# Kernel optimization log

Hardware: AMD Instinct MI355X
Metric: run time of the kernel (lower is better)

Reference implementation:

```python
import jax, jax.numpy as jnp
import numpy as np

D = 16      # input_dim (state dimension)
H = 64      # hidden width
B = 32768   # batch size


def setup_inputs() -> dict:
    key = jax.random.key(0)
    ks = jax.random.split(key, 16)
    inp = {
        "ts": jnp.arange(3, dtype=jnp.float32),          # output times [0, 1, 2]
        "x0": jax.random.normal(ks[0], (B, D), jnp.float32),
    }
    dims = [(D, H), (H, H), (H, H), (H, D)]
    i = 1
    for l, (din, dout) in enumerate(dims):
        inp[f"W{l}"] = jax.random.normal(ks[i], (din, dout), jnp.float32) / np.sqrt(din).astype(np.float32)
        inp[f"b{l}"] = jnp.zeros((dout,), jnp.float32)
        inp[f"g{l}"] = jax.random.normal(ks[i + 1], (dout,), jnp.float32) * 0.1   # hyper_gate weight (Linear(1,dout))
        inp[f"gb{l}"] = jnp.zeros((dout,), jnp.float32)                            # hyper_gate bias
        inp[f"hb{l}"] = jax.random.normal(ks[i + 2], (dout,), jnp.float32) * 0.1   # hyper_bias weight (no bias)
        i += 3
    return inp


def reference(ts, x0,
              W0, b0, g0, gb0, hb0,
              W1, b1, g1, gb1, hb1,
              W2, b2, g2, gb2, hb2,
              W3, b3, g3, gb3, hb3):
    layers = [(W0, b0, g0, gb0, hb0), (W1, b1, g1, gb1, hb1),
              (W2, b2, g2, gb2, hb2), (W3, b3, g3, gb3, hb3)]
    n_layers = len(layers)

    def odenet(t, x):
        # ConcatSquashLinear: (x@W + b) * sigmoid(t*g + gb) + t*hb, tanh between layers
        h = x
        for l, (W, b, g, gb, hb) in enumerate(layers):
            h = (h @ W + b) * jax.nn.sigmoid(t * g + gb) + t * hb
            if l < n_layers - 1:
                h = jnp.tanh(h)
        return h

    def odefunc(t, z):
        # z: [B, D+2]; last two channels accumulate log-det and kinetic energy
        x = z[:, :D]
        f = lambda xx: odenet(t, xx)
        dx = f(x)
        # exact divergence = trace of Jacobian, via D forward-mode JVPs
        eye = jnp.eye(D, dtype=x.dtype)
        Jv = jax.vmap(lambda e: jax.jvp(f, (x,), (jnp.broadcast_to(e, x.shape),))[1])(eye)  # [D, B, D]
        dl = jnp.einsum('ibi->b', Jv)                  # trace per sample
        dv = 0.5 * jnp.sum(dx * dx, axis=1)            # kinetic energy density
        return jnp.concatenate([dx, dl[:, None], dv[:, None]], axis=1)

    z0 = jnp.pad(x0, ((0, 0), (0, 2)))  # F.pad(x0, (0,2)) with zeros

    def rk4_step(z, t_pair):
        t0, t1 = t_pair
        h = t1 - t0
        k1 = odefunc(t0, z)
        k2 = odefunc(t0 + 0.5 * h, z + 0.5 * h * k1)
        k3 = odefunc(t0 + 0.5 * h, z + 0.5 * h * k2)
        k4 = odefunc(t1, z + h * k3)
        zn = z + (h / 6.0) * (k1 + 2.0 * k2 + 2.0 * k3 + k4)
        return zn, zn

    _, zs_tail = jax.lax.scan(rk4_step, z0, (ts[:-1], ts[1:]))
    zs = jnp.concatenate([z0[None], zs_tail], axis=0)   # [T, B, D+2]

    xs = zs[:, :, :-2]
    log_det = zs[-1, :, -2]
    loss_L = jnp.abs(zs[-1, :, -1])
    return xs, log_det, loss_L, jnp.zeros_like(loss_L)
```

## Files before the change

kernel.cpp:

```cpp
#include <hip/hip_runtime.h>

#define NB 32768
#define DD 16
#define HH 64
#define EPB 16

typedef __attribute__((ext_vector_type(8))) short short8;
typedef __attribute__((ext_vector_type(2))) float f32x2;
typedef __attribute__((ext_vector_type(4))) float f32x4;
typedef __attribute__((ext_vector_type(4))) unsigned uint4v;

union Frag { short8 s; uint4v u; unsigned d[4]; };

struct Params {
  const float *ts, *x0;
  const float *W0,*b0,*g0,*gb0,*hb0;
  const float *W1,*b1,*g1,*gb1,*hb1;
  const float *W2,*b2,*g2,*gb2,*hb2;
  const float *W3,*b3,*g3,*gb3,*hb3;
  float *out;
};

__device__ __forceinline__ float bfs(unsigned short u){
  return __uint_as_float(((unsigned)u)<<16);
}
__device__ __forceinline__ unsigned short f2bf(float f){
  unsigned u=__float_as_uint(f);
  return (unsigned short)((u + 0x7FFFu + ((u>>16)&1u))>>16);
}
__device__ __forceinline__ unsigned pk2bf(float lo, float hi){
  unsigned a=__float_as_uint(lo)+0x8000u;
  unsigned b=__float_as_uint(hi)+0x8000u;
  return __builtin_amdgcn_perm(b, a, 0x07060302u);
}
__device__ __forceinline__ unsigned short f2bf1(float f){
  return (unsigned short)((__float_as_uint(f)+0x8000u)>>16);
}
__device__ __forceinline__ float sigm(float u){
  return __builtin_amdgcn_rcpf(1.0f+__builtin_amdgcn_exp2f(-1.44269504f*u));
}
#define WV() __builtin_amdgcn_wave_barrier()
#define MFMA(A,B,C) __builtin_amdgcn_mfma_f32_16x16x32_bf16((A),(B),(C),0,0,0)

__device__ __forceinline__ void fwd_epi(const f32x4& c, float tcur,
    const float4 sc,
    unsigned short* __restrict__ hdst, unsigned short* __restrict__ sdst,
    int jw, int q)
{
  const float gate = sigm(tcur*sc.x+sc.y);
  const float gk   = gate*2.88539008f;
  const float tbk  = (tcur*sc.z)*2.88539008f;
  const float g4   = 4.0f*gate;
  const f32x2 c01={c[0],c[1]}, c23={c[2],c[3]};
  const f32x2 pre01 = c01*gk + tbk;
  const f32x2 pre23 = c23*gk + tbk;
  const f32x2 e01={__builtin_amdgcn_exp2f(pre01[0]),__builtin_amdgcn_exp2f(pre01[1])};
  const f32x2 e23={__builtin_amdgcn_exp2f(pre23[0]),__builtin_amdgcn_exp2f(pre23[1])};
  const f32x2 d01=e01+1.0f, d23=e23+1.0f;
  const f32x2 rc01={__builtin_amdgcn_rcpf(d01[0]),__builtin_amdgcn_rcpf(d01[1])};
  const f32x2 rc23={__builtin_amdgcn_rcpf(d23[0]),__builtin_amdgcn_rcpf(d23[1])};
  const f32x2 th01 = rc01*-2.0f + 1.0f;
  const f32x2 th23 = rc23*-2.0f + 1.0f;
  const f32x2 om01 = 1.0f - rc01, om23 = 1.0f - rc23;
  const f32x2 sv01 = (rc01*g4)*om01, sv23 = (rc23*g4)*om23;
  const int el0=q*4;
  hdst[(el0+0)*72+jw]=f2bf1(th01[0]);
  hdst[(el0+1)*72+jw]=f2bf1(th01[1]);
  hdst[(el0+2)*72+jw]=f2bf1(th23[0]);
  hdst[(el0+3)*72+jw]=f2bf1(th23[1]);
  sdst[(el0+0)*72+jw]=f2bf1(sv01[0]);
  sdst[(el0+1)*72+jw]=f2bf1(sv01[1]);
  sdst[(el0+2)*72+jw]=f2bf1(sv23[0]);
  sdst[(el0+3)*72+jw]=f2bf1(sv23[1]);
}

__device__ __forceinline__ void fwd_epi0(const f32x4& c, float tcur,
    const float4 sc,
    unsigned short* __restrict__ hdst, float* __restrict__ sdstf,
    int jw, int q)
{
  const float gate = sigm(tcur*sc.x+sc.y);
  const float gk   = gate*2.88539008f;
  const float tbk  = (tcur*sc.z)*2.88539008f;
  const float g4   = 4.0f*gate;
  const f32x2 c01={c[0],c[1]}, c23={c[2],c[3]};
  const f32x2 pre01 = c01*gk + tbk;
  const f32x2 pre23 = c23*gk + tbk;
  const f32x2 e01={__builtin_amdgcn_exp2f(pre01[0]),__builtin_amdgcn_exp2f(pre01[1])};
  const f32x2 e23={__builtin_amdgcn_exp2f(pre23[0]),__builtin_amdgcn_exp2f(pre23[1])};
  const f32x2 d01=e01+1.0f, d23=e23+1.0f;
  const f32x2 rc01={__builtin_amdgcn_rcpf(d01[0]),__builtin_amdgcn_rcpf(d01[1])};
  const f32x2 rc23={__builtin_amdgcn_rcpf(d23[0]),__builtin_amdgcn_rcpf(d23[1])};
  const f32x2 th01 = rc01*-2.0f + 1.0f;
  const f32x2 th23 = rc23*-2.0f + 1.0f;
  const f32x2 om01 = 1.0f - rc01, om23 = 1.0f - rc23;
  const f32x2 sv01 = (rc01*g4)*om01, sv23 = (rc23*g4)*om23;
  const int el0=q*4;
  hdst[(el0+0)*72+jw]=f2bf1(th01[0]);
  hdst[(el0+1)*72+jw]=f2bf1(th01[1]);
  hdst[(el0+2)*72+jw]=f2bf1(th23[0]);
  hdst[(el0+3)*72+jw]=f2bf1(th23[1]);
  sdstf[(el0+0)*72+jw]=sv01[0];
  sdstf[(el0+1)*72+jw]=sv01[1];
  sdstf[(el0+2)*72+jw]=sv23[0];
  sdstf[(el0+3)*72+jw]=sv23[1];
}

__global__ __launch_bounds__(256,3) void traj_kernel(Params p){
  __shared__ __align__(16) float w0f[DD][72];
  __shared__ __align__(16) float w3tt[HH][20];
  __shared__ __align__(16) unsigned short w0t[HH][16];
  __shared__ __align__(16) unsigned short b3f[2][64][8];
  __shared__ __align__(16) unsigned short w2tf[2][4][64][8];
  __shared__ __align__(16) float4 lscA[3][64];
  __shared__ __align__(16) float4 lsc3[16];
  __shared__ __align__(16) unsigned short xh[DD][16];
  __shared__ __align__(16) unsigned short xl[DD][16];
  __shared__ __align__(16) unsigned short hbh[2][EPB][72];
  __shared__ __align__(16) float sb0f[EPB][72];
  __shared__ __align__(16) unsigned short sb12[2][EPB][72];
  __shared__ __align__(16) float sig3w[4][DD];
  __shared__ __align__(16) float dxs[4][4][17];
  __shared__ __align__(16) unsigned short vt[4][DD][72];

  const int tid = threadIdx.x;
  const int e   = tid>>4;
  const int a   = tid&15;
  const int wv  = tid>>6;
  const int lane= tid&63;
  const int m   = lane&15;
  const int q   = lane>>4;
  const int b   = blockIdx.x*EPB + e;
  const int jw  = wv*16 + m;

  short8 f1fr[2], f2fr[2];
  short8 b1fr[2][4];
  {
    #pragma unroll
    for(int kk=0;kk<2;++kk){
      #pragma unroll
      for(int j=0;j<8;++j){
        const int k=kk*32+q*8+j;
        f1fr[kk][j]=(short)f2bf(p.W1[k*HH+jw]);
        f2fr[kk][j]=(short)f2bf(p.W2[k*HH+jw]);
      }
      #pragma unroll
      for(int nt=0;nt<4;++nt){
        #pragma unroll
        for(int j=0;j<8;++j){
          const int k=kk*32+q*8+j;
          b1fr[kk][nt][j]=(short)f2bf(p.W1[k*HH+4*m+nt]);
        }
      }
    }
  }

  for(int idx=tid; idx<DD*HH; idx+=256) w0f[idx>>6][idx&63]=p.W0[idx];
  for(int idx=tid; idx<HH*DD; idx+=256) w3tt[idx>>4][idx&15]=p.W3[idx];
  for(int idx=tid; idx<HH*16; idx+=256){
    const int c_=idx>>4, k=idx&15;
    w0t[c_][k]=f2bf(p.W0[k*HH+c_]);
  }
  for(int idx=tid; idx<1024; idx+=256){
    const int kk=idx>>9, ln=(idx>>3)&63, j=idx&7;
    const int k=kk*32+(ln>>4)*8+j;
    b3f[kk][ln][j]=f2bf(p.W3[k*DD+(ln&15)]);
  }
  for(int idx=tid; idx<4096; idx+=256){
    const int j=idx&7, ln=(idx>>3)&63, nt=(idx>>9)&3, kk=idx>>11;
    const int k=kk*32+((ln>>4)&3)*8+j;
    w2tf[kk][nt][ln][j]=f2bf(p.W2[k*HH+4*(ln&15)+nt]);
  }
  if(tid<64)            lscA[0][tid]    =make_float4(p.g0[tid],p.gb0[tid],p.hb0[tid],p.b0[tid]);
  else if(tid<128)      lscA[1][tid-64] =make_float4(p.g1[tid-64],p.gb1[tid-64],p.hb1[tid-64],p.b1[tid-64]);
  else if(tid<192)      lscA[2][tid-128]=make_float4(p.g2[tid-128],p.gb2[tid-128],p.hb2[tid-128],p.b2[tid-128]);
  else if(tid<208)      lsc3[tid-192]   =make_float4(p.g3[tid-192],p.gb3[tid-192],p.hb3[tid-192],p.b3[tid-192]);
  __syncthreads();

  float zbx = p.x0[b*DD+a];
  p.out[b*DD+a]=zbx;
  float trp[4]={0.f,0.f,0.f,0.f};
  float dvp=0.f;

  #pragma unroll 1
  for(int step=0; step<2; ++step){
    const float t0=p.ts[step], t1=p.ts[step+1];
    const float hs=t1-t0;
    float dzx=0.f;
    float zwx=zbx;
    #pragma unroll 1
    for(int stage=0; stage<4; ++stage){
      const float cin=(stage==0)?0.f:((stage==3)?1.f:0.5f);
      const float tcur=t0+cin*hs;
      const float wg=(stage==0||stage==3)?1.f:2.f;
      const float fs=hs*(1.f/6.f)*wg;
      const float fs5=0.5f*fs;

      {
        const unsigned ux=__float_as_uint(zwx);
        xh[e][a]=(unsigned short)(ux>>16);
        xl[e][a]=f2bf1(zwx-__uint_as_float(ux&0xFFFF0000u));
      }
      __syncthreads();

      float4 sc0=lscA[0][jw];
      f32x4 c={sc0.w,sc0.w,sc0.w,sc0.w};
      {
        short8 f0fr=short8{0,0,0,0,0,0,0,0};
        short8 ah=f0fr, al=f0fr;
        if(q<2){
          f0fr=*reinterpret_cast<const short8*>(&w0t[jw][q*8]);
          ah  =*reinterpret_cast<const short8*>(&xh[m][q*8]);
          al  =*reinterpret_cast<const short8*>(&xl[m][q*8]);
        }
        c=MFMA(ah,f0fr,c); c=MFMA(al,f0fr,c);
      }
      fwd_epi0(c,tcur,sc0,&hbh[0][0][0],&sb0f[0][0],jw,q);
      __syncthreads();

      float4 sc1=lscA[1][jw];
      c=f32x4{sc1.w,sc1.w,sc1.w,sc1.w};
      #pragma unroll
      for(int kk=0;kk<2;++kk){
        const short8 ah=*reinterpret_cast<const short8*>(&hbh[0][m][kk*32+q*8]);
        c=MFMA(ah,f1fr[kk],c);
      }
      fwd_epi(c,tcur,sc1,&hbh[1][0][0],&sb12[0][0][0],jw,q);
      __syncthreads();

      float4 sc2=lscA[2][jw];
      c=f32x4{sc2.w,sc2.w,sc2.w,sc2.w};
      #pragma unroll
      for(int kk=0;kk<2;++kk){
        const short8 ah=*reinterpret_cast<const short8*>(&hbh[1][m][kk*32+q*8]);
        c=MFMA(ah,f2fr[kk],c);
      }
      fwd_epi(c,tcur,sc2,&hbh[0][0][0],&sb12[1][0][0],jw,q);
      __syncthreads();

      float4 sc3=lsc3[m];
      c=f32x4{sc3.w,sc3.w,sc3.w,sc3.w};
      #pragma unroll
      for(int kk=0;kk<2;++kk){
        const short8 bf3=*reinterpret_cast<const short8*>(&b3f[kk][lane][0]);
        const short8 ah=*reinterpret_cast<const short8*>(&hbh[0][m][kk*32+q*8]);
        c=MFMA(ah,bf3,c);
      }
      const float gate3=sigm(tcur*sc3.x+sc3.y);
      const float tb3=tcur*sc3.z;
      if(q==wv){
        #pragma unroll
        for(int r=0;r<4;++r)
          dxs[wv][r][m]=c[r]*gate3+tb3;
      }
      if(q==0) sig3w[wv][m]=gate3;
      WV();
      const float dxk=dxs[wv][q][m];
      dvp += fs5*dxk*dxk;

      f32x2 tf2[4][2];
      {
        const f32x4 sg4=*reinterpret_cast<const f32x4*>(&sig3w[wv][q*4]);
        const f32x2 sgA={sg4[0],sg4[1]}, sgB={sg4[2],sg4[3]};
        #pragma unroll
        for(int nt=0;nt<4;++nt){
          const f32x4 w4=*reinterpret_cast<const f32x4*>(&w3tt[4*m+nt][q*4]);
          tf2[nt][0]=sgA*f32x2{w4[0],w4[1]};
          tf2[nt][1]=sgB*f32x2{w4[2],w4[3]};
        }
      }

      #pragma unroll
      for(int el=0; el<4; ++el){
        const int ee=wv*4+el;
        Frag a0[2];
        #pragma unroll
        for(int kk=0;kk<2;++kk){
          const f32x4 wa=*reinterpret_cast<const f32x4*>(&w0f[m][kk*32+q*8]);
          const f32x4 wb=*reinterpret_cast<const f32x4*>(&w0f[m][kk*32+q*8+4]);
          const f32x4 sa=*reinterpret_cast<const f32x4*>(&sb0f[ee][kk*32+q*8]);
          const f32x4 sc_=*reinterpret_cast<const f32x4*>(&sb0f[ee][kk*32+q*8+4]);
          a0[kk].d[0]=pk2bf(wa[0]*sa[0], wa[1]*sa[1]);
          a0[kk].d[1]=pk2bf(wa[2]*sa[2], wa[3]*sa[3]);
          a0[kk].d[2]=pk2bf(wb[0]*sc_[0], wb[1]*sc_[1]);
          a0[kk].d[3]=pk2bf(wb[2]*sc_[2], wb[3]*sc_[3]);
        }
        #pragma unroll
        for(int np=0; np<2; ++np){
          f32x4 cA={0,0,0,0}, cB={0,0,0,0};
          #pragma unroll
          for(int kk=0;kk<2;++kk){
            cA=MFMA(a0[kk].s,b1fr[kk][2*np  ],cA);
            cB=MFMA(a0[kk].s,b1fr[kk][2*np+1],cB);
          }
          const unsigned s1d=*reinterpret_cast<const unsigned*>(&sb12[0][ee][4*m+2*np]);
          const float sA_=__uint_as_float(s1d<<16), sB_=__uint_as_float(s1d&0xFFFF0000u);
          const f32x4 prA=cA*sA_, prB=cB*sB_;
          #pragma unroll
          for(int r=0;r<4;++r)
            *reinterpret_cast<unsigned*>(&vt[wv][q*4+r][4*m+2*np])=pk2bf(prA[r],prB[r]);
        }
        WV();
        short8 a2[2];
        #pragma unroll
        for(int kk=0;kk<2;++kk)
          a2[kk]=*reinterpret_cast<const short8*>(&vt[wv][m][kk*32+q*8]);
        float tr=0.f;
        #pragma unroll
        for(int np=0; np<2; ++np){
          f32x4 cA={0,0,0,0}, cB={0,0,0,0};
          #pragma unroll
          for(int kk=0;kk<2;++kk){
            const short8 bA=*reinterpret_cast<const short8*>(&w2tf[kk][2*np  ][lane][0]);
            const short8 bB=*reinterpret_cast<const short8*>(&w2tf[kk][2*np+1][lane][0]);
            cA=MFMA(a2[kk],bA,cA);
            cB=MFMA(a2[kk],bB,cB);
          }
          const unsigned s2d=*reinterpret_cast<const unsigned*>(&sb12[1][ee][4*m+2*np]);
          const float s20=__uint_as_float(s2d<<16), s21=__uint_as_float(s2d&0xFFFF0000u);
          const f32x2 tA = f32x2{cA[0],cA[1]}*tf2[2*np  ][0] + f32x2{cA[2],cA[3]}*tf2[2*np  ][1];
          const f32x2 tB = f32x2{cB[0],cB[1]}*tf2[2*np+1][0] + f32x2{cB[2],cB[3]}*tf2[2*np+1][1];
          tr += (tA[0]+tA[1])*s20 + (tB[0]+tB[1])*s21;
        }
        trp[el] += fs*tr;
        WV();
      }

      dzx += fs*dxk;
      const float cn=(stage==2)?1.f:0.5f;
      if(stage<3) zwx=zbx+cn*hs*dxk;
    }
    zbx += dzx;
    p.out[(step+1)*(NB*DD)+b*DD+a]=zbx;
  }

  #pragma unroll
  for(int el=0; el<4; ++el){
    float v=trp[el];
    #pragma unroll
    for(int mk=32;mk>=1;mk>>=1) v+=__shfl_xor(v,mk,64);
    if(lane==el) p.out[3*NB*DD + blockIdx.x*EPB + wv*4 + el]=v;
  }
  {
    float v=dvp;
    #pragma unroll
    for(int mk=8;mk>=1;mk>>=1) v+=__shfl_xor(v,mk,16);
    if(a==0){
      p.out[3*NB*DD+NB+b]=fabsf(v);
      p.out[3*NB*DD+2*NB+b]=0.f;
    }
  }
}

extern "C" void kernel_launch(void* const* d_in, const int* in_sizes, int n_in,
                              void* d_out, int out_size, void* d_ws, size_t ws_size,
                              hipStream_t stream){
  Params p;
  p.ts  = (const float*)d_in[0];
  p.x0  = (const float*)d_in[1];
  p.W0  = (const float*)d_in[2];  p.b0 =(const float*)d_in[3];
  p.g0  = (const float*)d_in[4];  p.gb0=(const float*)d_in[5];  p.hb0=(const float*)d_in[6];
  p.W1  = (const float*)d_in[7];  p.b1 =(const float*)d_in[8];
  p.g1  = (const float*)d_in[9];  p.gb1=(const float*)d_in[10]; p.hb1=(const float*)d_in[11];
  p.W2  = (const float*)d_in[12]; p.b2 =(const float*)d_in[13];
  p.g2  = (const float*)d_in[14]; p.gb2=(const float*)d_in[15]; p.hb2=(const float*)d_in[16];
  p.W3  = (const float*)d_in[17]; p.b3 =(const float*)d_in[18];
  p.g3  = (const float*)d_in[19]; p.gb3=(const float*)d_in[20]; p.hb3=(const float*)d_in[21];
  p.out = (float*)d_out;
  hipLaunchKernelGGL(traj_kernel, dim3(NB/EPB), dim3(256), 0, stream, p);
}
```

Baseline: 238.0 us.

## Hold W2/W3 MFMA fragments in registers and alias activation and JVP LDS buffers

Moves the W2-transpose and W3 B-fragments from shared memory into per-lane registers, which removes the LDS reads inside the per-element JVP loop. The hbh activation buffers and the vt JVP buffer now share one region, with an extra block barrier added before the JVP phase to make the reuse safe. Row padding of w0f and sb0f changes from 72 to 76 floats to reduce bank conflicts. Launch bounds drop from 3 to 2 blocks per CU so the extra registers fit, which lowers occupancy.

```diff
diff --git a/kernel.cpp b/kernel.cpp
--- a/kernel.cpp
+++ b/kernel.cpp
@@ -100,28 +100,25 @@
   hdst[(el0+1)*72+jw]=f2bf1(th01[1]);
   hdst[(el0+2)*72+jw]=f2bf1(th23[0]);
   hdst[(el0+3)*72+jw]=f2bf1(th23[1]);
-  sdstf[(el0+0)*72+jw]=sv01[0];
-  sdstf[(el0+1)*72+jw]=sv01[1];
-  sdstf[(el0+2)*72+jw]=sv23[0];
-  sdstf[(el0+3)*72+jw]=sv23[1];
-}
-
-__global__ __launch_bounds__(256,3) void traj_kernel(Params p){
-  __shared__ __align__(16) float w0f[DD][72];
+  sdstf[(el0+0)*76+jw]=sv01[0];
+  sdstf[(el0+1)*76+jw]=sv01[1];
+  sdstf[(el0+2)*76+jw]=sv23[0];
+  sdstf[(el0+3)*76+jw]=sv23[1];
+}
+
+__global__ __launch_bounds__(256,2) void traj_kernel(Params p){
+  __shared__ __align__(16) float w0f[DD][76];
   __shared__ __align__(16) float w3tt[HH][20];
   __shared__ __align__(16) unsigned short w0t[HH][16];
-  __shared__ __align__(16) unsigned short b3f[2][64][8];
-  __shared__ __align__(16) unsigned short w2tf[2][4][64][8];
   __shared__ __align__(16) float4 lscA[3][64];
   __shared__ __align__(16) float4 lsc3[16];
   __shared__ __align__(16) unsigned short xh[DD][16];
   __shared__ __align__(16) unsigned short xl[DD][16];
-  __shared__ __align__(16) unsigned short hbh[2][EPB][72];
-  __shared__ __align__(16) float sb0f[EPB][72];
+  __shared__ __align__(16) unsigned short hvt[4][DD][72];
+  __shared__ __align__(16) float sb0f[EPB][76];
   __shared__ __align__(16) unsigned short sb12[2][EPB][72];
   __shared__ __align__(16) float sig3w[4][DD];
   __shared__ __align__(16) float dxs[4][4][17];
-  __shared__ __align__(16) unsigned short vt[4][DD][72];
 
   const int tid = threadIdx.x;
   const int e   = tid>>4;
@@ -135,6 +132,8 @@
 
   short8 f1fr[2], f2fr[2];
   short8 b1fr[2][4];
+  short8 w2r[2][4];
+  short8 b3r[2];
   {
     #pragma unroll
     for(int kk=0;kk<2;++kk){
@@ -143,6 +142,7 @@
         const int k=kk*32+q*8+j;
         f1fr[kk][j]=(short)f2bf(p.W1[k*HH+jw]);
         f2fr[kk][j]=(short)f2bf(p.W2[k*HH+jw]);
+        b3r[kk][j]=(short)f2bf(p.W3[k*DD+m]);
       }
       #pragma unroll
       for(int nt=0;nt<4;++nt){
@@ -150,6 +150,7 @@
         for(int j=0;j<8;++j){
           const int k=kk*32+q*8+j;
           b1fr[kk][nt][j]=(short)f2bf(p.W1[k*HH+4*m+nt]);
+          w2r[kk][nt][j]=(short)f2bf(p.W2[k*HH+4*m+nt]);
         }
       }
     }
@@ -160,16 +161,6 @@
   for(int idx=tid; idx<HH*16; idx+=256){
     const int c_=idx>>4, k=idx&15;
     w0t[c_][k]=f2bf(p.W0[k*HH+c_]);
-  }
-  for(int idx=tid; idx<1024; idx+=256){
-    const int kk=idx>>9, ln=(idx>>3)&63, j=idx&7;
-    const int k=kk*32+(ln>>4)*8+j;
-    b3f[kk][ln][j]=f2bf(p.W3[k*DD+(ln&15)]);
-  }
-  for(int idx=tid; idx<4096; idx+=256){
-    const int j=idx&7, ln=(idx>>3)&63, nt=(idx>>9)&3, kk=idx>>11;
-    const int k=kk*32+((ln>>4)&3)*8+j;
-    w2tf[kk][nt][ln][j]=f2bf(p.W2[k*HH+4*(ln&15)+nt]);
   }
   if(tid<64)            lscA[0][tid]    =make_float4(p.g0[tid],p.gb0[tid],p.hb0[tid],p.b0[tid]);
   else if(tid<128)      lscA[1][tid-64] =make_float4(p.g1[tid-64],p.gb1[tid-64],p.hb1[tid-64],p.b1[tid-64]);
@@ -215,36 +206,35 @@
         }
         c=MFMA(ah,f0fr,c); c=MFMA(al,f0fr,c);
       }
-      fwd_epi0(c,tcur,sc0,&hbh[0][0][0],&sb0f[0][0],jw,q);
+      fwd_epi0(c,tcur,sc0,&hvt[0][0][0],&sb0f[0][0],jw,q);
       __syncthreads();
 
       float4 sc1=lscA[1][jw];
       c=f32x4{sc1.w,sc1.w,sc1.w,sc1.w};
       #pragma unroll
       for(int kk=0;kk<2;++kk){
-        const short8 ah=*reinterpret_cast<const short8*>(&hbh[0][m][kk*32+q*8]);
+        const short8 ah=*reinterpret_cast<const short8*>(&hvt[0][m][kk*32+q*8]);
         c=MFMA(ah,f1fr[kk],c);
       }
-      fwd_epi(c,tcur,sc1,&hbh[1][0][0],&sb12[0][0][0],jw,q);
+      fwd_epi(c,tcur,sc1,&hvt[1][0][0],&sb12[0][0][0],jw,q);
       __syncthreads();
 
       float4 sc2=lscA[2][jw];
       c=f32x4{sc2.w,sc2.w,sc2.w,sc2.w};
       #pragma unroll
       for(int kk=0;kk<2;++kk){
-        const short8 ah=*reinterpret_cast<const short8*>(&hbh[1][m][kk*32+q*8]);
+        const short8 ah=*reinterpret_cast<const short8*>(&hvt[1][m][kk*32+q*8]);
         c=MFMA(ah,f2fr[kk],c);
       }
-      fwd_epi(c,tcur,sc2,&hbh[0][0][0],&sb12[1][0][0],jw,q);
+      fwd_epi(c,tcur,sc2,&hvt[0][0][0],&sb12[1][0][0],jw,q);
       __syncthreads();
 
       float4 sc3=lsc3[m];
       c=f32x4{sc3.w,sc3.w,sc3.w,sc3.w};
       #pragma unroll
       for(int kk=0;kk<2;++kk){
-        const short8 bf3=*reinterpret_cast<const short8*>(&b3f[kk][lane][0]);
-        const short8 ah=*reinterpret_cast<const short8*>(&hbh[0][m][kk*32+q*8]);
-        c=MFMA(ah,bf3,c);
+        const short8 ah=*reinterpret_cast<const short8*>(&hvt[0][m][kk*32+q*8]);
+        c=MFMA(ah,b3r[kk],c);
       }
       const float gate3=sigm(tcur*sc3.x+sc3.y);
       const float tb3=tcur*sc3.z;
@@ -269,6 +259,8 @@
           tf2[nt][1]=sgB*f32x2{w4[2],w4[3]};
         }
       }
+
+      __syncthreads();
 
       #pragma unroll
       for(int el=0; el<4; ++el){
@@ -298,23 +290,21 @@
           const f32x4 prA=cA*sA_, prB=cB*sB_;
           #pragma unroll
           for(int r=0;r<4;++r)
-            *reinterpret_cast<unsigned*>(&vt[wv][q*4+r][4*m+2*np])=pk2bf(prA[r],prB[r]);
+            *reinterpret_cast<unsigned*>(&hvt[wv][q*4+r][4*m+2*np])=pk2bf(prA[r],prB[r]);
         }
         WV();
         short8 a2[2];
         #pragma unroll
         for(int kk=0;kk<2;++kk)
-          a2[kk]=*reinterpret_cast<const short8*>(&vt[wv][m][kk*32+q*8]);
+          a2[kk]=*reinterpret_cast<const short8*>(&hvt[wv][m][kk*32+q*8]);
         float tr=0.f;
         #pragma unroll
         for(int np=0; np<2; ++np){
           f32x4 cA={0,0,0,0}, cB={0,0,0,0};
           #pragma unroll
           for(int kk=0;kk<2;++kk){
-            const short8 bA=*reinterpret_cast<const short8*>(&w2tf[kk][2*np  ][lane][0]);
-            const short8 bB=*reinterpret_cast<const short8*>(&w2tf[kk][2*np+1][lane][0]);
-            cA=MFMA(a2[kk],bA,cA);
-            cB=MFMA(a2[kk],bB,cB);
+            cA=MFMA(a2[kk],w2r[kk][2*np  ],cA);
+            cB=MFMA(a2[kk],w2r[kk][2*np+1],cB);
           }
           const unsigned s2d=*reinterpret_cast<const unsigned*>(&sb12[1][ee][4*m+2*np]);
           const float s20=__uint_as_float(s2d<<16), s21=__uint_as_float(s2d&0xFFFF0000u);
```

After: 241.3 us. No clear change (+1.4%).

## Compute transposed layer-1 JVP tile so MFMA output feeds next MFMA in registers

Applied to the files above, without the earlier changes.

Swaps the operands of the layer-1 Jacobian MFMA so its accumulator layout matches the A-fragment layout needed by the layer-2 MFMA. The vt shared-memory staging buffer, its LDS writes and reads, and two wave barriers per element go away. W2 fragments are re-permuted along k to match the new register ordering. Row padding of the w0f and sb0f arrays also changes from 72 to 76 floats to reduce LDS bank conflicts.

```diff
diff --git a/kernel.cpp b/kernel.cpp
--- a/kernel.cpp
+++ b/kernel.cpp
@@ -100,14 +100,14 @@
   hdst[(el0+1)*72+jw]=f2bf1(th01[1]);
   hdst[(el0+2)*72+jw]=f2bf1(th23[0]);
   hdst[(el0+3)*72+jw]=f2bf1(th23[1]);
-  sdstf[(el0+0)*72+jw]=sv01[0];
-  sdstf[(el0+1)*72+jw]=sv01[1];
-  sdstf[(el0+2)*72+jw]=sv23[0];
-  sdstf[(el0+3)*72+jw]=sv23[1];
+  sdstf[(el0+0)*76+jw]=sv01[0];
+  sdstf[(el0+1)*76+jw]=sv01[1];
+  sdstf[(el0+2)*76+jw]=sv23[0];
+  sdstf[(el0+3)*76+jw]=sv23[1];
 }
 
 __global__ __launch_bounds__(256,3) void traj_kernel(Params p){
-  __shared__ __align__(16) float w0f[DD][72];
+  __shared__ __align__(16) float w0f[DD][76];
   __shared__ __align__(16) float w3tt[HH][20];
   __shared__ __align__(16) unsigned short w0t[HH][16];
   __shared__ __align__(16) unsigned short b3f[2][64][8];
@@ -117,11 +117,10 @@
   __shared__ __align__(16) unsigned short xh[DD][16];
   __shared__ __align__(16) unsigned short xl[DD][16];
   __shared__ __align__(16) unsigned short hbh[2][EPB][72];
-  __shared__ __align__(16) float sb0f[EPB][72];
+  __shared__ __align__(16) float sb0f[EPB][76];
   __shared__ __align__(16) unsigned short sb12[2][EPB][72];
   __shared__ __align__(16) float sig3w[4][DD];
   __shared__ __align__(16) float dxs[4][4][17];
-  __shared__ __align__(16) unsigned short vt[4][DD][72];
 
   const int tid = threadIdx.x;
   const int e   = tid>>4;
@@ -134,7 +133,7 @@
   const int jw  = wv*16 + m;
 
   short8 f1fr[2], f2fr[2];
-  short8 b1fr[2][4];
+  short8 w1gA[4][2];
   {
     #pragma unroll
     for(int kk=0;kk<2;++kk){
@@ -145,11 +144,11 @@
         f2fr[kk][j]=(short)f2bf(p.W2[k*HH+jw]);
       }
       #pragma unroll
-      for(int nt=0;nt<4;++nt){
+      for(int g=0;g<4;++g){
         #pragma unroll
         for(int j=0;j<8;++j){
           const int k=kk*32+q*8+j;
-          b1fr[kk][nt][j]=(short)f2bf(p.W1[k*HH+4*m+nt]);
+          w1gA[g][kk][j]=(short)f2bf(p.W1[k*HH + g*16 + m]);
         }
       }
     }
@@ -168,7 +167,9 @@
   }
   for(int idx=tid; idx<4096; idx+=256){
     const int j=idx&7, ln=(idx>>3)&63, nt=(idx>>9)&3, kk=idx>>11;
-    const int k=kk*32+((ln>>4)&3)*8+j;
+    const int qq=(ln>>4)&3;
+    const int t=kk*8+j;
+    const int k=16*(t>>2) + 4*qq + (t&3);
     w2tf[kk][nt][ln][j]=f2bf(p.W2[k*HH+4*(ln&15)+nt]);
   }
   if(tid<64)            lscA[0][tid]    =make_float4(p.g0[tid],p.gb0[tid],p.hb0[tid],p.b0[tid]);
@@ -285,26 +286,25 @@
           a0[kk].d[2]=pk2bf(wb[0]*sc_[0], wb[1]*sc_[1]);
           a0[kk].d[3]=pk2bf(wb[2]*sc_[2], wb[3]*sc_[3]);
         }
-        #pragma unroll
-        for(int np=0; np<2; ++np){
-          f32x4 cA={0,0,0,0}, cB={0,0,0,0};
-          #pragma unroll
-          for(int kk=0;kk<2;++kk){
-            cA=MFMA(a0[kk].s,b1fr[kk][2*np  ],cA);
-            cB=MFMA(a0[kk].s,b1fr[kk][2*np+1],cB);
-          }
-          const unsigned s1d=*reinterpret_cast<const unsigned*>(&sb12[0][ee][4*m+2*np]);
-          const float sA_=__uint_as_float(s1d<<16), sB_=__uint_as_float(s1d&0xFFFF0000u);
-          const f32x4 prA=cA*sA_, prB=cB*sB_;
-          #pragma unroll
-          for(int r=0;r<4;++r)
-            *reinterpret_cast<unsigned*>(&vt[wv][q*4+r][4*m+2*np])=pk2bf(prA[r],prB[r]);
-        }
-        WV();
-        short8 a2[2];
-        #pragma unroll
-        for(int kk=0;kk<2;++kk)
-          a2[kk]=*reinterpret_cast<const short8*>(&vt[wv][m][kk*32+q*8]);
+        f32x4 dt0={0,0,0,0}, dt1={0,0,0,0}, dt2={0,0,0,0}, dt3={0,0,0,0};
+        #pragma unroll
+        for(int kk=0;kk<2;++kk){
+          dt0=MFMA(w1gA[0][kk], a0[kk].s, dt0);
+          dt1=MFMA(w1gA[1][kk], a0[kk].s, dt1);
+          dt2=MFMA(w1gA[2][kk], a0[kk].s, dt2);
+          dt3=MFMA(w1gA[3][kk], a0[kk].s, dt3);
+        }
+        const unsigned* s1p=reinterpret_cast<const unsigned*>(&sb12[0][ee][0]);
+        Frag a2[2];
+        #pragma unroll
+        for(int g=0; g<4; ++g){
+          const unsigned da=s1p[8*g+2*q], db=s1p[8*g+2*q+1];
+          const f32x4 s={__uint_as_float(da<<16),__uint_as_float(da&0xFFFF0000u),
+                         __uint_as_float(db<<16),__uint_as_float(db&0xFFFF0000u)};
+          const f32x4 v=(g==0?dt0:(g==1?dt1:(g==2?dt2:dt3)))*s;
+          a2[g>>1].d[(g&1)*2+0]=pk2bf(v[0],v[1]);
+          a2[g>>1].d[(g&1)*2+1]=pk2bf(v[2],v[3]);
+        }
         float tr=0.f;
         #pragma unroll
         for(int np=0; np<2; ++np){
@@ -313,8 +313,8 @@
           for(int kk=0;kk<2;++kk){
             const short8 bA=*reinterpret_cast<const short8*>(&w2tf[kk][2*np  ][lane][0]);
             const short8 bB=*reinterpret_cast<const short8*>(&w2tf[kk][2*np+1][lane][0]);
-            cA=MFMA(a2[kk],bA,cA);
-            cB=MFMA(a2[kk],bB,cB);
+            cA=MFMA(a2[kk].s,bA,cA);
+            cB=MFMA(a2[kk].s,bB,cB);
           }
           const unsigned s2d=*reinterpret_cast<const unsigned*>(&sb12[1][ee][4*m+2*np]);
           const float s20=__uint_as_float(s2d<<16), s21=__uint_as_float(s2d&0xFFFF0000u);
@@ -323,7 +323,6 @@
           tr += (tA[0]+tA[1])*s20 + (tB[0]+tB[1])*s21;
         }
         trp[el] += fs*tr;
-        WV();
       }
 
       dzx += fs*dxk;
```

Result: slower. 245.9 us (+3.3%).
